# Performance work log

Hardware: AMD Instinct MI355X
Metric: run time of the kernel (lower is better)

## Reference

```python
import jax, jax.numpy as jnp
import numpy as np

MARGIN = 0.5

def setup_inputs() -> dict:
    key = jax.random.key(0)
    k1, k2 = jax.random.split(key)
    n, d, n_classes = 8192, 512, 1024
    embedding = jax.random.normal(k1, (n, d), dtype=jnp.float32)
    label = jax.random.randint(k2, (n,), 0, n_classes, dtype=jnp.int64)
    return {"embedding": embedding, "label": label}


def reference(embedding, label):
    # sim_mat[i, j] = <e_i, e_j>
    n = embedding.shape[0]
    sim = embedding @ embedding.T  # [n, n]
    same = label[:, None] == label[None, :]  # [n, n] bool
    # per-row positive pairs: same label AND sim < 1; loss contrib (1 - sim)
    pos_mask = same & (sim < 1.0)
    # per-row negative pairs (hard mining): diff label AND sim > margin; loss contrib sim
    neg_mask = (~same) & (sim > MARGIN)
    pos_loss = jnp.sum(jnp.where(pos_mask, 1.0 - sim, 0.0))
    neg_loss = jnp.sum(jnp.where(neg_mask, sim, 0.0))
    loss = (pos_loss + neg_loss) / n
    return (loss, 0, 0)
```

## Files before the change

kernel.cpp:

```cpp
#include <hip/hip_runtime.h>
#include <hip/hip_bf16.h>


typedef int   i32x4 __attribute__((ext_vector_type(4)));
typedef float f32x4 __attribute__((ext_vector_type(4)));

#define N_EMB 8192
#define D_EMB 512
#define BM    128
#define BKB   64
#define KT    (D_EMB / BKB)
#define TILES (N_EMB / BM)
#define NBLK  (TILES * (TILES + 1) / 2)
#define MARGIN_F 0.5f
#define QSCALE 24.0f
#define DEQ    (1.0f / (QSCALE * QSCALE))
#define ABYT  (BM * BKB)

__device__ __forceinline__ void gll16(const void* g, void* l) {
    __builtin_amdgcn_global_load_lds(
        (const __attribute__((address_space(1))) void*)g,
        (__attribute__((address_space(3))) void*)l,
        16 , 0 , 0 );
}

__global__ __launch_bounds__(256) void quant_kernel(const float* __restrict__ in,
                                                    int4* __restrict__ out, int n16) {
    int i = blockIdx.x * blockDim.x + threadIdx.x;
    if (i >= n16) return;
    const float4* p = reinterpret_cast<const float4*>(in) + i * 4;
    int4 o;
    int* po = reinterpret_cast<int*>(&o);
#pragma unroll
    for (int j = 0; j < 4; ++j) {
        float4 v = p[j];
        int b0 = (int)rintf(fminf(fmaxf(v.x * QSCALE, -127.f), 127.f));
        int b1 = (int)rintf(fminf(fmaxf(v.y * QSCALE, -127.f), 127.f));
        int b2 = (int)rintf(fminf(fmaxf(v.z * QSCALE, -127.f), 127.f));
        int b3 = (int)rintf(fminf(fmaxf(v.w * QSCALE, -127.f), 127.f));
        po[j] = (b0 & 255) | ((b1 & 255) << 8) | ((b2 & 255) << 16) | ((b3 & 255) << 24);
    }
    out[i] = o;
}

__global__ __launch_bounds__(256) void loss_kernel(const char* __restrict__ E8,
                                                   const int* __restrict__ label,
                                                   float* __restrict__ partials) {
    const int bid = blockIdx.x;
    const int t = (bid & 7) * (NBLK / 8) + (bid >> 3);

    int tr = (int)(64.5f - sqrtf(4160.25f - 2.0f * (float)t));
    while ((tr + 1) * TILES - ((tr + 1) * tr) / 2 <= t) ++tr;
    while (tr * TILES - (tr * (tr - 1)) / 2 > t) --tr;
    const int tc = tr + (t - (tr * TILES - (tr * (tr - 1)) / 2));

    __shared__ char  lds[3][2 * ABYT];
    __shared__ float red[4];

    const int tid  = threadIdx.x;
    const int wid  = tid >> 6, lane = tid & 63;
    const int wrow = wid >> 1, wcol = wid & 1;
    const int fr   = lane & 15;
    const int kq   = lane >> 4;
    const int row0 = tr * BM, col0 = tc * BM;

    const int s1 = tid + 256;
    const char* gA0 = E8 + (size_t)(row0 + (tid >> 2)) * D_EMB + ((tid & 3) << 4);
    const char* gA1 = E8 + (size_t)(row0 + (s1 >> 2)) * D_EMB + ((s1 & 3) << 4);
    const char* gB0 = E8 + (size_t)(col0 + (tid >> 2)) * D_EMB + ((tid & 3) << 4);
    const char* gB1 = E8 + (size_t)(col0 + (s1 >> 2)) * D_EMB + ((s1 & 3) << 4);
    const int dA0 = tid << 4,          dA1 = s1 << 4;
    const int dB0 = ABYT + (tid << 4), dB1 = ABYT + (s1 << 4);

    i32x4 acc[4][4] = {};

    gll16(gA0,       lds[0] + dA0); gll16(gA1,       lds[0] + dA1);
    gll16(gB0,       lds[0] + dB0); gll16(gB1,       lds[0] + dB1);
    gll16(gA0 + BKB, lds[1] + dA0); gll16(gA1 + BKB, lds[1] + dA1);
    gll16(gB0 + BKB, lds[1] + dB0); gll16(gB1 + BKB, lds[1] + dB1);

    char* rd  = lds[0];
    char* pre = lds[1];
    char* wr  = lds[2];

#pragma unroll 1
    for (int kt = 0; kt < KT; ++kt) {
        if (kt < KT - 1) {
            asm volatile("s_waitcnt vmcnt(4)" ::: "memory");
        } else {
            asm volatile("s_waitcnt vmcnt(0)" ::: "memory");
        }
        __builtin_amdgcn_s_barrier();

        if (kt + 2 < KT) {
            const int k2 = (kt + 2) * BKB;
            gll16(gA0 + k2, wr + dA0); gll16(gA1 + k2, wr + dA1);
            gll16(gB0 + k2, wr + dB0); gll16(gB1 + k2, wr + dB1);
        }
        __builtin_amdgcn_sched_barrier(0);

        i32x4 a[4], b[4];
#pragma unroll
        for (int m = 0; m < 4; ++m)
            a[m] = *reinterpret_cast<const i32x4*>(
                &rd[(wrow * 64 + m * 16 + fr) * BKB + (kq << 4)]);
#pragma unroll
        for (int n = 0; n < 4; ++n)
            b[n] = *reinterpret_cast<const i32x4*>(
                &rd[ABYT + (wcol * 64 + n * 16 + fr) * BKB + (kq << 4)]);
#pragma unroll
        for (int m = 0; m < 4; ++m)
#pragma unroll
            for (int n = 0; n < 4; ++n)
                acc[m][n] = __builtin_amdgcn_mfma_i32_16x16x64_i8(a[m], b[n], acc[m][n], 0, 0, 0);

        char* tmp = rd; rd = pre; pre = wr; wr = tmp;
    }

    float local = 0.f;
    int lj[4];
#pragma unroll
    for (int n = 0; n < 4; ++n) lj[n] = label[col0 + wcol * 64 + n * 16 + fr];
    const int rb = kq << 2;
#pragma unroll
    for (int m = 0; m < 4; ++m) {
#pragma unroll
        for (int r = 0; r < 4; ++r) {
            const int li = label[row0 + wrow * 64 + m * 16 + rb + r];
#pragma unroll
            for (int n = 0; n < 4; ++n) {
                const float s = (float)acc[m][n][r] * DEQ;
                if (li == lj[n]) {
                    if (s < 1.0f) local += 1.0f - s;
                } else if (s > MARGIN_F) {
                    local += s;
                }
            }
        }
    }
    if (tr != tc) local *= 2.0f;

#pragma unroll
    for (int off = 32; off > 0; off >>= 1) local += __shfl_xor(local, off);
    if (lane == 0) red[wid] = local;
    __syncthreads();
    if (tid == 0) partials[t] = red[0] + red[1] + red[2] + red[3];
}

__global__ __launch_bounds__(256) void reduce_kernel(const float* __restrict__ partials,
                                                     float* __restrict__ out, int nb) {
    float s = 0.f;
    for (int i = threadIdx.x; i < nb; i += 256) s += partials[i];
#pragma unroll
    for (int off = 32; off > 0; off >>= 1) s += __shfl_xor(s, off);
    __shared__ float red[4];
    if ((threadIdx.x & 63) == 0) red[threadIdx.x >> 6] = s;
    __syncthreads();
    if (threadIdx.x == 0) {
        out[0] = (red[0] + red[1] + red[2] + red[3]) * (1.0f / (float)N_EMB);
        out[1] = 0.f;
        out[2] = 0.f;
    }
}

extern "C" void kernel_launch(void* const* d_in, const int* in_sizes, int n_in,
                              void* d_out, int out_size, void* d_ws, size_t ws_size,
                              hipStream_t stream) {
    const float* emb   = (const float*)d_in[0];
    const int*   label = (const int*)d_in[1];
    float*       out   = (float*)d_out;

    char*  E8      = (char*)d_ws;
    float* partial = (float*)((char*)d_ws + (size_t)N_EMB * D_EMB);

    const int n16 = N_EMB * D_EMB / 16;
    quant_kernel<<<(n16 + 255) / 256, 256, 0, stream>>>(emb, (int4*)E8, n16);

    loss_kernel<<<NBLK, 256, 0, stream>>>(E8, label, partial);

    reduce_kernel<<<1, 256, 0, stream>>>(partial, out, NBLK);
}
```

Before: 48.62 us.

## Double the int8 K-tile to 128 with XOR-swizzled LDS and double buffering

Raises the per-stage K slice from 64 to 128 bytes, so the loop runs 4 iterations instead of 8. It moves from triple to double buffering and uses 8 loads per thread per stage. Each thread's 16-byte chunk is placed in LDS with an XOR swizzle on the row index, and reads apply the same swizzle. This is meant to remove the LDS bank conflicts caused by the old 64-byte row stride, and each stage now issues two MFMAs per accumulator. The trade-offs: LDS per block grows from 48KB to 64KB, which can cut resident blocks per CU, and loads only overlap one stage ahead.

```diff
diff --git a/kernel.cpp b/kernel.cpp
--- a/kernel.cpp
+++ b/kernel.cpp
@@ -8,7 +8,7 @@
 #define N_EMB 8192
 #define D_EMB 512
 #define BM    128
-#define BKB   64
+#define BKB   128
 #define KT    (D_EMB / BKB)
 #define TILES (N_EMB / BM)
 #define NBLK  (TILES * (TILES + 1) / 2)
@@ -54,7 +54,7 @@
     while (tr * TILES - (tr * (tr - 1)) / 2 > t) --tr;
     const int tc = tr + (t - (tr * TILES - (tr * (tr - 1)) / 2));
 
-    __shared__ char  lds[3][2 * ABYT];
+    __shared__ char  lds[2][2 * ABYT];
     __shared__ float red[4];
 
     const int tid  = threadIdx.x;
@@ -64,57 +64,69 @@
     const int kq   = lane >> 4;
     const int row0 = tr * BM, col0 = tc * BM;
 
-    const int s1 = tid + 256;
-    const char* gA0 = E8 + (size_t)(row0 + (tid >> 2)) * D_EMB + ((tid & 3) << 4);
-    const char* gA1 = E8 + (size_t)(row0 + (s1 >> 2)) * D_EMB + ((s1 & 3) << 4);
-    const char* gB0 = E8 + (size_t)(col0 + (tid >> 2)) * D_EMB + ((tid & 3) << 4);
-    const char* gB1 = E8 + (size_t)(col0 + (s1 >> 2)) * D_EMB + ((s1 & 3) << 4);
-    const int dA0 = tid << 4,          dA1 = s1 << 4;
-    const int dB0 = ABYT + (tid << 4), dB1 = ABYT + (s1 << 4);
+    const int swb = (((tid & 7) ^ ((tid >> 3) & 7)) << 4);
+    const int rbase = tid >> 3;
+    const char* gA[4]; const char* gB[4];
+    int dA[4], dB[4];
+#pragma unroll
+    for (int j = 0; j < 4; ++j) {
+        const int r = rbase + 32 * j;
+        gA[j] = E8 + (size_t)(row0 + r) * D_EMB + swb;
+        gB[j] = E8 + (size_t)(col0 + r) * D_EMB + swb;
+        dA[j] = (tid << 4) + (j << 12);
+        dB[j] = ABYT + (tid << 4) + (j << 12);
+    }
 
     i32x4 acc[4][4] = {};
 
-    gll16(gA0,       lds[0] + dA0); gll16(gA1,       lds[0] + dA1);
-    gll16(gB0,       lds[0] + dB0); gll16(gB1,       lds[0] + dB1);
-    gll16(gA0 + BKB, lds[1] + dA0); gll16(gA1 + BKB, lds[1] + dA1);
-    gll16(gB0 + BKB, lds[1] + dB0); gll16(gB1 + BKB, lds[1] + dB1);
+    const int c0 = ((kq ^ (fr & 7)) << 4);
 
-    char* rd  = lds[0];
-    char* pre = lds[1];
-    char* wr  = lds[2];
+#pragma unroll
+    for (int j = 0; j < 4; ++j) { gll16(gA[j],       lds[0] + dA[j]);
+                                  gll16(gB[j],       lds[0] + dB[j]); }
+#pragma unroll
+    for (int j = 0; j < 4; ++j) { gll16(gA[j] + BKB, lds[1] + dA[j]);
+                                  gll16(gB[j] + BKB, lds[1] + dB[j]); }
 
 #pragma unroll 1
     for (int kt = 0; kt < KT; ++kt) {
-        if (kt < KT - 1) {
-            asm volatile("s_waitcnt vmcnt(4)" ::: "memory");
+        if (kt == 0) {
+            asm volatile("s_waitcnt vmcnt(8)" ::: "memory");
         } else {
             asm volatile("s_waitcnt vmcnt(0)" ::: "memory");
         }
         __builtin_amdgcn_s_barrier();
 
-        if (kt + 2 < KT) {
-            const int k2 = (kt + 2) * BKB;
-            gll16(gA0 + k2, wr + dA0); gll16(gA1 + k2, wr + dA1);
-            gll16(gB0 + k2, wr + dB0); gll16(gB1 + k2, wr + dB1);
+        if (kt + 1 < KT && kt > 0) {
+            const int k1 = (kt + 1) * BKB;
+            char* w = lds[(kt + 1) & 1];
+#pragma unroll
+            for (int j = 0; j < 4; ++j) { gll16(gA[j] + k1, w + dA[j]);
+                                          gll16(gB[j] + k1, w + dB[j]); }
         }
         __builtin_amdgcn_sched_barrier(0);
 
-        i32x4 a[4], b[4];
+        const char* rd = lds[kt & 1];
+        i32x4 a[4][2], b[4][2];
 #pragma unroll
-        for (int m = 0; m < 4; ++m)
-            a[m] = *reinterpret_cast<const i32x4*>(
-                &rd[(wrow * 64 + m * 16 + fr) * BKB + (kq << 4)]);
+        for (int m = 0; m < 4; ++m) {
+            const int base = (wrow * 64 + m * 16 + fr) << 7;
+            a[m][0] = *reinterpret_cast<const i32x4*>(&rd[base + c0]);
+            a[m][1] = *reinterpret_cast<const i32x4*>(&rd[base + (c0 ^ 64)]);
+        }
 #pragma unroll
-        for (int n = 0; n < 4; ++n)
-            b[n] = *reinterpret_cast<const i32x4*>(
-                &rd[ABYT + (wcol * 64 + n * 16 + fr) * BKB + (kq << 4)]);
+        for (int n = 0; n < 4; ++n) {
+            const int base = ABYT + ((wcol * 64 + n * 16 + fr) << 7);
+            b[n][0] = *reinterpret_cast<const i32x4*>(&rd[base + c0]);
+            b[n][1] = *reinterpret_cast<const i32x4*>(&rd[base + (c0 ^ 64)]);
+        }
 #pragma unroll
         for (int m = 0; m < 4; ++m)
 #pragma unroll
-            for (int n = 0; n < 4; ++n)
-                acc[m][n] = __builtin_amdgcn_mfma_i32_16x16x64_i8(a[m], b[n], acc[m][n], 0, 0, 0);
-
-        char* tmp = rd; rd = pre; pre = wr; wr = tmp;
+            for (int n = 0; n < 4; ++n) {
+                acc[m][n] = __builtin_amdgcn_mfma_i32_16x16x64_i8(a[m][0], b[n][0], acc[m][n], 0, 0, 0);
+                acc[m][n] = __builtin_amdgcn_mfma_i32_16x16x64_i8(a[m][1], b[n][1], acc[m][n], 0, 0, 0);
+            }
     }
 
     float local = 0.f;
```

Result: slower. 55.87 us (+14.9%).

## Swizzle LDS tiles and restructure K-loop with prefetch-after-read and priority MFMA phase

Applied to the files above, without the earlier changes.

Applies an XOR swizzle to the 16-byte chunk position within each 64-byte LDS row, on both the global-to-LDS loads and the fragment reads, to reduce LDS bank conflicts. The K loop is fully unrolled. Each iteration now reads its fragments, issues the next prefetch, then waits and barriers before a priority-raised MFMA block followed by a second barrier. The aim is to overlap loads with compute and give MFMA issue priority, at the cost of an extra barrier per phase and larger unrolled code.

```diff
diff --git a/kernel.cpp b/kernel.cpp
--- a/kernel.cpp
+++ b/kernel.cpp
@@ -8,14 +8,14 @@
 #define N_EMB 8192
 #define D_EMB 512
 #define BM    128
-#define BKB   64
-#define KT    (D_EMB / BKB)
+#define HKB   64
+#define NPH   (D_EMB / HKB)
 #define TILES (N_EMB / BM)
 #define NBLK  (TILES * (TILES + 1) / 2)
 #define MARGIN_F 0.5f
 #define QSCALE 24.0f
 #define DEQ    (1.0f / (QSCALE * QSCALE))
-#define ABYT  (BM * BKB)
+#define HBYT  (BM * HKB)
 
 __device__ __forceinline__ void gll16(const void* g, void* l) {
     __builtin_amdgcn_global_load_lds(
@@ -54,7 +54,7 @@
     while (tr * TILES - (tr * (tr - 1)) / 2 > t) --tr;
     const int tc = tr + (t - (tr * TILES - (tr * (tr - 1)) / 2));
 
-    __shared__ char  lds[3][2 * ABYT];
+    __shared__ char  lds[3][2][HBYT];
     __shared__ float red[4];
 
     const int tid  = threadIdx.x;
@@ -64,57 +64,60 @@
     const int kq   = lane >> 4;
     const int row0 = tr * BM, col0 = tc * BM;
 
-    const int s1 = tid + 256;
-    const char* gA0 = E8 + (size_t)(row0 + (tid >> 2)) * D_EMB + ((tid & 3) << 4);
-    const char* gA1 = E8 + (size_t)(row0 + (s1 >> 2)) * D_EMB + ((s1 & 3) << 4);
-    const char* gB0 = E8 + (size_t)(col0 + (tid >> 2)) * D_EMB + ((tid & 3) << 4);
-    const char* gB1 = E8 + (size_t)(col0 + (s1 >> 2)) * D_EMB + ((s1 & 3) << 4);
-    const int dA0 = tid << 4,          dA1 = s1 << 4;
-    const int dB0 = ABYT + (tid << 4), dB1 = ABYT + (s1 << 4);
+    const int sw = (((tid & 3) ^ ((tid >> 2) & 3)) << 4);
+    const int r0 = tid >> 2, r1 = 64 + (tid >> 2);
+    const char* gA0 = E8 + (size_t)(row0 + r0) * D_EMB + sw;
+    const char* gA1 = E8 + (size_t)(row0 + r1) * D_EMB + sw;
+    const char* gB0 = E8 + (size_t)(col0 + r0) * D_EMB + sw;
+    const char* gB1 = E8 + (size_t)(col0 + r1) * D_EMB + sw;
+    const int d0 = tid << 4;
+    const int d1 = (tid + 256) << 4;
 
     i32x4 acc[4][4] = {};
 
-    gll16(gA0,       lds[0] + dA0); gll16(gA1,       lds[0] + dA1);
-    gll16(gB0,       lds[0] + dB0); gll16(gB1,       lds[0] + dB1);
-    gll16(gA0 + BKB, lds[1] + dA0); gll16(gA1 + BKB, lds[1] + dA1);
-    gll16(gB0 + BKB, lds[1] + dB0); gll16(gB1 + BKB, lds[1] + dB1);
+    const int psw = ((kq ^ (fr & 3)) << 4);
 
-    char* rd  = lds[0];
-    char* pre = lds[1];
-    char* wr  = lds[2];
+    gll16(gA0,       &lds[0][0][d0]); gll16(gA1,       &lds[0][0][d1]);
+    gll16(gB0,       &lds[0][1][d0]); gll16(gB1,       &lds[0][1][d1]);
+    gll16(gA0 + HKB, &lds[1][0][d0]); gll16(gA1 + HKB, &lds[1][0][d1]);
+    gll16(gB0 + HKB, &lds[1][1][d0]); gll16(gB1 + HKB, &lds[1][1][d1]);
+    asm volatile("s_waitcnt vmcnt(4)" ::: "memory");
+    __builtin_amdgcn_s_barrier();
 
-#pragma unroll 1
-    for (int kt = 0; kt < KT; ++kt) {
-        if (kt < KT - 1) {
-            asm volatile("s_waitcnt vmcnt(4)" ::: "memory");
-        } else {
-            asm volatile("s_waitcnt vmcnt(0)" ::: "memory");
-        }
-        __builtin_amdgcn_s_barrier();
-
-        if (kt + 2 < KT) {
-            const int k2 = (kt + 2) * BKB;
-            gll16(gA0 + k2, wr + dA0); gll16(gA1 + k2, wr + dA1);
-            gll16(gB0 + k2, wr + dB0); gll16(gB1 + k2, wr + dB1);
-        }
-        __builtin_amdgcn_sched_barrier(0);
-
+#pragma unroll
+    for (int p = 0; p < NPH; ++p) {
+        const int rg = p % 3;
         i32x4 a[4], b[4];
 #pragma unroll
         for (int m = 0; m < 4; ++m)
             a[m] = *reinterpret_cast<const i32x4*>(
-                &rd[(wrow * 64 + m * 16 + fr) * BKB + (kq << 4)]);
+                &lds[rg][0][((wrow * 64 + m * 16 + fr) << 6) + psw]);
 #pragma unroll
         for (int n = 0; n < 4; ++n)
             b[n] = *reinterpret_cast<const i32x4*>(
-                &rd[ABYT + (wcol * 64 + n * 16 + fr) * BKB + (kq << 4)]);
+                &lds[rg][1][((wcol * 64 + n * 16 + fr) << 6) + psw]);
+        if (p + 2 < NPH) {
+            const int rg2 = (p + 2) % 3;
+            const int ko  = (p + 2) * HKB;
+            gll16(gA0 + ko, &lds[rg2][0][d0]); gll16(gA1 + ko, &lds[rg2][0][d1]);
+            gll16(gB0 + ko, &lds[rg2][1][d0]); gll16(gB1 + ko, &lds[rg2][1][d1]);
+        }
+        if (p < NPH - 2) {
+            asm volatile("s_waitcnt vmcnt(4)" ::: "memory");
+        } else if (p == NPH - 2) {
+            asm volatile("s_waitcnt vmcnt(0)" ::: "memory");
+        }
+        __builtin_amdgcn_s_barrier();
+        asm volatile("s_waitcnt lgkmcnt(0)" ::: "memory");
+        __builtin_amdgcn_sched_barrier(0);
+        __builtin_amdgcn_s_setprio(1);
 #pragma unroll
         for (int m = 0; m < 4; ++m)
 #pragma unroll
             for (int n = 0; n < 4; ++n)
                 acc[m][n] = __builtin_amdgcn_mfma_i32_16x16x64_i8(a[m], b[n], acc[m][n], 0, 0, 0);
-
-        char* tmp = rd; rd = pre; pre = wr; wr = tmp;
+        __builtin_amdgcn_s_setprio(0);
+        __builtin_amdgcn_s_barrier();
     }
 
     float local = 0.f;
```

Measured after the change: 46.15 us. 1.05x faster.

## Load MFMA operands directly from global memory, dropping LDS staging pipeline

Applied to the files above, without the earlier changes.

Removes the triple-buffered LDS pipeline (global_load_lds, waitcnt, barriers) and has each wave load its int8 A/B fragments straight from global memory in a fully unrolled K loop. The aim is to cut LDS traffic and barrier synchronisation, relying on L1/L2 caching because the quantized matrix (4 MB) fits in cache. In exchange, each wave issues redundant global loads, since waves sharing rows or columns each fetch their own copy. The compiler now also has to schedule and overlap these loads without explicit prefetching.

```diff
diff --git a/kernel.cpp b/kernel.cpp
--- a/kernel.cpp
+++ b/kernel.cpp
@@ -8,21 +8,11 @@
 #define N_EMB 8192
 #define D_EMB 512
 #define BM    128
-#define BKB   64
-#define KT    (D_EMB / BKB)
 #define TILES (N_EMB / BM)
 #define NBLK  (TILES * (TILES + 1) / 2)
 #define MARGIN_F 0.5f
 #define QSCALE 24.0f
 #define DEQ    (1.0f / (QSCALE * QSCALE))
-#define ABYT  (BM * BKB)
-
-__device__ __forceinline__ void gll16(const void* g, void* l) {
-    __builtin_amdgcn_global_load_lds(
-        (const __attribute__((address_space(1))) void*)g,
-        (__attribute__((address_space(3))) void*)l,
-        16 , 0 , 0 );
-}
 
 __global__ __launch_bounds__(256) void quant_kernel(const float* __restrict__ in,
                                                     int4* __restrict__ out, int n16) {
@@ -54,7 +44,6 @@
     while (tr * TILES - (tr * (tr - 1)) / 2 > t) --tr;
     const int tc = tr + (t - (tr * TILES - (tr * (tr - 1)) / 2));
 
-    __shared__ char  lds[3][2 * ABYT];
     __shared__ float red[4];
 
     const int tid  = threadIdx.x;
@@ -64,57 +53,31 @@
     const int kq   = lane >> 4;
     const int row0 = tr * BM, col0 = tc * BM;
 
-    const int s1 = tid + 256;
-    const char* gA0 = E8 + (size_t)(row0 + (tid >> 2)) * D_EMB + ((tid & 3) << 4);
-    const char* gA1 = E8 + (size_t)(row0 + (s1 >> 2)) * D_EMB + ((s1 & 3) << 4);
-    const char* gB0 = E8 + (size_t)(col0 + (tid >> 2)) * D_EMB + ((tid & 3) << 4);
-    const char* gB1 = E8 + (size_t)(col0 + (s1 >> 2)) * D_EMB + ((s1 & 3) << 4);
-    const int dA0 = tid << 4,          dA1 = s1 << 4;
-    const int dB0 = ABYT + (tid << 4), dB1 = ABYT + (s1 << 4);
+    const char* pa[4];
+    const char* pb[4];
+#pragma unroll
+    for (int m = 0; m < 4; ++m)
+        pa[m] = E8 + (size_t)(row0 + wrow * 64 + m * 16 + fr) * D_EMB + (kq << 4);
+#pragma unroll
+    for (int n = 0; n < 4; ++n)
+        pb[n] = E8 + (size_t)(col0 + wcol * 64 + n * 16 + fr) * D_EMB + (kq << 4);
 
     i32x4 acc[4][4] = {};
 
-    gll16(gA0,       lds[0] + dA0); gll16(gA1,       lds[0] + dA1);
-    gll16(gB0,       lds[0] + dB0); gll16(gB1,       lds[0] + dB1);
-    gll16(gA0 + BKB, lds[1] + dA0); gll16(gA1 + BKB, lds[1] + dA1);
-    gll16(gB0 + BKB, lds[1] + dB0); gll16(gB1 + BKB, lds[1] + dB1);
-
-    char* rd  = lds[0];
-    char* pre = lds[1];
-    char* wr  = lds[2];
-
-#pragma unroll 1
-    for (int kt = 0; kt < KT; ++kt) {
-        if (kt < KT - 1) {
-            asm volatile("s_waitcnt vmcnt(4)" ::: "memory");
-        } else {
-            asm volatile("s_waitcnt vmcnt(0)" ::: "memory");
-        }
-        __builtin_amdgcn_s_barrier();
-
-        if (kt + 2 < KT) {
-            const int k2 = (kt + 2) * BKB;
-            gll16(gA0 + k2, wr + dA0); gll16(gA1 + k2, wr + dA1);
-            gll16(gB0 + k2, wr + dB0); gll16(gB1 + k2, wr + dB1);
-        }
-        __builtin_amdgcn_sched_barrier(0);
-
+#pragma unroll
+    for (int k0 = 0; k0 < D_EMB; k0 += 64) {
         i32x4 a[4], b[4];
 #pragma unroll
         for (int m = 0; m < 4; ++m)
-            a[m] = *reinterpret_cast<const i32x4*>(
-                &rd[(wrow * 64 + m * 16 + fr) * BKB + (kq << 4)]);
+            a[m] = *reinterpret_cast<const i32x4*>(pa[m] + k0);
 #pragma unroll
         for (int n = 0; n < 4; ++n)
-            b[n] = *reinterpret_cast<const i32x4*>(
-                &rd[ABYT + (wcol * 64 + n * 16 + fr) * BKB + (kq << 4)]);
+            b[n] = *reinterpret_cast<const i32x4*>(pb[n] + k0);
 #pragma unroll
         for (int m = 0; m < 4; ++m)
 #pragma unroll
             for (int n = 0; n < 4; ++n)
                 acc[m][n] = __builtin_amdgcn_mfma_i32_16x16x64_i8(a[m], b[n], acc[m][n], 0, 0, 0);
-
-        char* tmp = rd; rd = pre; pre = wr; wr = tmp;
     }
 
     float local = 0.f;
```

After: 89.21 us. +83.5%, slower.
